# Kernel tuning notes

Hardware: AMD Instinct MI355X
Metric: run time of the kernel (lower is better)

Reference implementation:

```python
import jax, jax.numpy as jnp
import numpy as np

E = 128   # embedding_dim
H = 4     # num_heads
D = E * H # internal width = 512 (MHA head_dim = E)
B = 512
N = 128


def setup_inputs() -> dict:
    key = jax.random.key(0)
    ks = jax.random.split(key, 16)
    s = lambda fan_in: 1.0 / np.sqrt(fan_in)
    u = lambda k, shape, sc: jax.random.uniform(k, shape, jnp.float32, -sc, sc)
    inp = {
        "x": jax.random.normal(ks[0], (B, N, E), jnp.float32),
        "weights": jax.random.uniform(ks[1], (B, N, 1), jnp.float32),
        # self.embedding: Linear(E, D)
        "emb_W": u(ks[2], (D, E), s(E)), "emb_b": u(ks[3], (D,), s(E)),
        # outer W_q/W_k/W_v: Linear(D, D)
        "wq_W": u(ks[4], (D, D), s(D)), "wq_b": u(ks[5], (D,), s(D)),
        "wk_W": u(ks[6], (D, D), s(D)), "wk_b": u(ks[7], (D,), s(D)),
        "wv_W": u(ks[8], (D, D), s(D)), "wv_b": u(ks[9], (D,), s(D)),
        # nn.MultiheadAttention packed in-projection (out_proj is irrelevant:
        # its output is discarded, only att_weights are used)
        "in_proj_W": u(ks[10], (3 * D, D), s(D)),
        "in_proj_b": jnp.zeros((3 * D,), jnp.float32),
        # LayerNorm(D)
        "ln_g": jnp.ones((D,), jnp.float32), "ln_b": jnp.zeros((D,), jnp.float32),
        # self.out: Linear(D, E)
        "out_W": u(ks[11], (E, D), s(D)), "out_b": u(ks[12], (E,), s(D)),
    }
    return inp


def reference(x, weights, emb_W, emb_b, wq_W, wq_b, wk_W, wk_b, wv_W, wv_b,
              in_proj_W, in_proj_b, ln_g, ln_b, out_W, out_b):
    # x: [B, N, E] -> embedded [B, N, D]
    xe = x @ emb_W.T + emb_b
    # key_padding_mask: rows of xe that are all-zero
    pad = jnp.sum(jnp.abs(xe), axis=-1) == 0.0              # [B, N] bool

    # outer projections
    q_in = xe @ wq_W.T + wq_b
    k_in = xe @ wk_W.T + wk_b
    v_in = xe @ wv_W.T + wv_b                               # [B, N, D]

    # MHA internal packed in-projection
    Wq, Wk, Wv = in_proj_W[:D], in_proj_W[D:2 * D], in_proj_W[2 * D:]
    bq, bk, bv = in_proj_b[:D], in_proj_b[D:2 * D], in_proj_b[2 * D:]
    hd = D // H  # head_dim = E
    to_heads = lambda t: t.reshape(t.shape[0], t.shape[1], H, hd).transpose(0, 2, 1, 3)
    q = to_heads(q_in @ Wq.T + bq)                          # [B, H, N, hd]
    k = to_heads(k_in @ Wk.T + bk)

    scores = jnp.einsum('bhie,bhje->bhij', q, k) / jnp.sqrt(jnp.float32(hd))
    scores = jnp.where(pad[:, None, None, :], -jnp.inf, scores)
    attn = jax.nn.softmax(scores, axis=-1)                  # [B, H, N, N]
    att_weights = jnp.mean(attn, axis=1)                    # averaged over heads [B, N, N]

    # external reweighting + renormalization
    att_weights = att_weights * jnp.swapaxes(weights, -2, -1)  # [B,N,N]*[B,1,N]
    att_weights = att_weights / jnp.sum(att_weights, axis=-1, keepdims=True)

    # re-apply to outer V projection (MHA's own output is discarded)
    att_output = jnp.einsum('bij,bjd->bid', att_weights, v_in)

    h = xe + jax.nn.softplus(att_output)
    mu = jnp.mean(h, axis=-1, keepdims=True)
    var = jnp.mean((h - mu) ** 2, axis=-1, keepdims=True)
    h = (h - mu) / jnp.sqrt(var + 1e-5) * ln_g + ln_b
    return h @ out_W.T + out_b                              # [B, N, E]
```

## Files before the change

### kernel.cpp

```cpp
#include <hip/hip_runtime.h>
#include <stdint.h>


typedef __attribute__((ext_vector_type(8))) __bf16 bf16x8;
typedef __attribute__((ext_vector_type(8))) uint16_t u16x8;
typedef __attribute__((ext_vector_type(4))) float f32x4;

__device__ __forceinline__ float b2f(uint16_t h) {
  union { uint32_t u; float f; } c; c.u = ((uint32_t)h) << 16; return c.f;
}
__device__ __forceinline__ uint16_t f2b(float f) {
  union { float f; uint32_t u; } c; c.f = f;
  return (uint16_t)((c.u + 0x7fffu + ((c.u >> 16) & 1u)) >> 16);
}
__device__ __forceinline__ void gld16(void* lds, const void* g) {
  __builtin_amdgcn_global_load_lds(
      (const __attribute__((address_space(1))) uint32_t*)(g),
      (__attribute__((address_space(3))) uint32_t*)(lds),
      16, 0, 0);
}

#define MFMA16(a, b, c) __builtin_amdgcn_mfma_f32_16x16x32_bf16((a), (b), (c), 0, 0, 0)

__global__ __launch_bounds__(256) void pack_bf16(const float* __restrict__ in,
                                                 uint16_t* __restrict__ out, int n4) {
  int i = blockIdx.x * 256 + threadIdx.x;
  if (i >= n4) return;
  float4 v = ((const float4*)in)[i];
  ushort4 o;
  o.x = f2b(v.x); o.y = f2b(v.y); o.z = f2b(v.z); o.w = f2b(v.w);
  ((ushort4*)out)[i] = o;
}

__global__ __launch_bounds__(256) void pack_w6(
    const float* __restrict__ emb_W, const float* __restrict__ wq_W,
    const float* __restrict__ wk_W, const float* __restrict__ wv_W,
    const float* __restrict__ ipW, const float* __restrict__ out_W,
    uint16_t* __restrict__ embW2, uint16_t* __restrict__ wqW_bf,
    uint16_t* __restrict__ wkW_bf, uint16_t* __restrict__ Wvc,
    uint16_t* __restrict__ ip_bf, uint16_t* __restrict__ owW_bf) {
  int i = blockIdx.x * 256 + threadIdx.x;
  const float* src; uint16_t* dst; int off;
  if (i < 16384)       { src = emb_W; dst = embW2;  off = i; }
  else if (i < 81920)  { src = wq_W;  dst = wqW_bf; off = i - 16384; }
  else if (i < 147456) { src = wk_W;  dst = wkW_bf; off = i - 81920; }
  else if (i < 212992) { src = wv_W;  dst = Wvc;    off = i - 147456; }
  else if (i < 344064) { src = ipW;   dst = ip_bf;  off = i - 212992; }
  else if (i < 360448) { src = out_W; dst = owW_bf; off = i - 344064; }
  else return;
  float4 v = ((const float4*)src)[off];
  ushort4 o;
  o.x = f2b(v.x); o.y = f2b(v.y); o.z = f2b(v.z); o.w = f2b(v.w);
  ((ushort4*)dst)[off] = o;
}

__global__ __launch_bounds__(256) void bias_stage1(
    const float* __restrict__ wq_W, const float* __restrict__ wk_W,
    const float* __restrict__ wv_W, const float* __restrict__ emb_b,
    const float* __restrict__ wq_b, const float* __restrict__ wk_b,
    const float* __restrict__ wv_b,
    float* __restrict__ t1q, float* __restrict__ t1k, float* __restrict__ bve,
    float* __restrict__ pad_init, float* __restrict__ biasE) {
  const int gid = blockIdx.x * 256 + threadIdx.x;
  if (gid < 65536) pad_init[gid] = 0.f;
  if (gid < 512) biasE[gid] = emb_b[gid];
  const int t = threadIdx.x, l = t & 63, w = t >> 6;
  const int sel = blockIdx.x >> 7;
  const int row = (blockIdx.x & 127) * 4 + w;
  const float* Wbig = sel == 0 ? wq_W : (sel == 1 ? wk_W : wv_W);
  const float* b2   = sel == 0 ? wq_b : (sel == 1 ? wk_b : wv_b);
  float* out        = sel == 0 ? t1q  : (sel == 1 ? t1k  : bve);
  float s = 0.f;
  #pragma unroll
  for (int j = 0; j < 8; ++j) {
    int c = j * 64 + l;
    s += Wbig[(size_t)row * 512 + c] * emb_b[c];
  }
  #pragma unroll
  for (int m = 1; m < 64; m <<= 1) s += __shfl_xor(s, m);
  if (l == 0) out[row] = s + b2[row];
}

__global__ __launch_bounds__(256) void bias_stage2(
    const float* __restrict__ ipW, const float* __restrict__ ipb,
    const float* __restrict__ t1q, const float* __restrict__ t1k,
    float* __restrict__ bqe, float* __restrict__ bke) {
  const int t = threadIdx.x, l = t & 63, w = t >> 6;
  const int sel = blockIdx.x >> 7;
  const int row = (blockIdx.x & 127) * 4 + w;
  const float* Wbig = ipW + (size_t)sel * 262144;
  const float* b1   = sel == 0 ? t1q : t1k;
  const float* b2   = ipb + sel * 512;
  float* out        = sel == 0 ? bqe : bke;
  float s = 0.f;
  #pragma unroll
  for (int j = 0; j < 8; ++j) {
    int c = j * 64 + l;
    s += Wbig[(size_t)row * 512 + c] * b1[c];
  }
  #pragma unroll
  for (int m = 1; m < 64; m <<= 1) s += __shfl_xor(s, m);
  if (l == 0) out[row] = s + b2[row];
}

template <int BIAS_MODE, bool PAD_ACC>
__global__ __launch_bounds__(256) void gemm_btp_kernel(
    const uint16_t* __restrict__ A, long long sA,
    const uint16_t* __restrict__ W, long long sW,
    const float* __restrict__ bias, long long sBias,
    uint16_t* __restrict__ C, long long sC,
    int mIter, float* __restrict__ padout) {
  __shared__ uint16_t Ws[2][128 * 64];
  __shared__ uint16_t As[2][128 * 64];
  const int t = threadIdx.x, l = t & 63, w = t >> 6;
  const int wr = w >> 1, wc = w & 1, l15 = l & 15, hi = l >> 4;
  const int gx = gridDim.x, gy = gridDim.y;
  const int nwg = gx * gy * gridDim.z;
  const int lin = blockIdx.x + gx * (blockIdx.y + gy * blockIdx.z);
  const int cpx = nwg >> 3;
  const int sw = (nwg & 7) ? lin : ((lin & 7) * cpx + (lin >> 3));
  const int ntile = sw % gx;
  const int rest = sw / gx;
  const int mg = rest % gy, bz = rest / gy;
  const uint16_t* Ab = A + (size_t)bz * sA;
  const uint16_t* Wb = W + (size_t)bz * sW;
  uint16_t* Cb = C + (size_t)bz * sC;
  const float* biasb = bias + (size_t)bz * sBias;
  const int srow = t >> 3;
  const int schunk = (t & 7) * 8;
  const int gchunk = (((t & 7) ^ (srow & 7)) * 8);
  const int rowB0 = ntile * 128;
  #pragma unroll
  for (int kt = 0; kt < 2; ++kt)
    #pragma unroll
    for (int i = 0; i < 4; ++i) {
      const int r = i * 32 + srow;
      gld16(&Ws[kt][r * 64 + schunk], Wb + (size_t)(rowB0 + r) * 128 + kt * 64 + gchunk);
    }
  auto stageA = [&](int u) {
    const int rowA0 = (mg * mIter + (u >> 1)) * 128;
    const int kb = (u & 1) << 6;
    #pragma unroll
    for (int i = 0; i < 4; ++i) {
      const int r = i * 32 + srow;
      gld16(&As[u & 1][r * 64 + schunk], Ab + (size_t)(rowA0 + r) * 128 + kb + gchunk);
    }
  };
  const int rsw = (l15 & 7);
  stageA(0);
  const int U = mIter * 2;
  f32x4 acc[4][4];
  for (int u = 0; u < U; ++u) {
    const int kt = u & 1;
    if (kt == 0) {
      #pragma unroll
      for (int m = 0; m < 4; ++m)
        #pragma unroll
        for (int n = 0; n < 4; ++n) acc[m][n] = (f32x4){0.f, 0.f, 0.f, 0.f};
    }
    if (u + 1 < U) {
      stageA(u + 1);
      asm volatile("s_waitcnt vmcnt(4)" ::: "memory");
    } else {
      asm volatile("s_waitcnt vmcnt(0)" ::: "memory");
    }
    __builtin_amdgcn_s_barrier();
    asm volatile("" ::: "memory");
    #pragma unroll
    for (int ks = 0; ks < 2; ++ks) {
      const int gck = ((ks * 4 + hi) ^ rsw) * 8;
      bf16x8 a[4], bb[4];
      #pragma unroll
      for (int m = 0; m < 4; ++m)
        a[m] = *(const bf16x8*)&As[kt][(wr * 64 + m * 16 + l15) * 64 + gck];
      #pragma unroll
      for (int n = 0; n < 4; ++n)
        bb[n] = *(const bf16x8*)&Ws[kt][(wc * 64 + n * 16 + l15) * 64 + gck];
      #pragma unroll
      for (int m = 0; m < 4; ++m)
        #pragma unroll
        for (int n = 0; n < 4; ++n) acc[m][n] = MFMA16(a[m], bb[n], acc[m][n]);
    }
    asm volatile("" ::: "memory");
    __builtin_amdgcn_s_barrier();
    if (kt == 1) {
      const int rowA0 = (mg * mIter + (u >> 1)) * 128;
      #pragma unroll
      for (int m = 0; m < 4; ++m) {
        const int row = rowA0 + wr * 64 + m * 16 + hi * 4;
        float padp[4] = {0.f, 0.f, 0.f, 0.f};
        #pragma unroll
        for (int n = 0; n < 4; ++n) {
          const int col = rowB0 + wc * 64 + n * 16 + l15;
          float bv = 0.f;
          if constexpr (BIAS_MODE == 1) bv = biasb[col];
          #pragma unroll
          for (int r = 0; r < 4; ++r) {
            float rv = acc[m][n][r] + bv;
            if constexpr (PAD_ACC) padp[r] += fabsf(rv);
            Cb[(size_t)(row + r) * 512 + col] = f2b(rv);
          }
        }
        if constexpr (PAD_ACC) {
          if (bz == 0) {
            #pragma unroll
            for (int r = 0; r < 4; ++r) {
              float s2 = padp[r];
              s2 += __shfl_xor(s2, 1); s2 += __shfl_xor(s2, 2);
              s2 += __shfl_xor(s2, 4); s2 += __shfl_xor(s2, 8);
              if (l15 == 0) atomicAdd(padout + row + r, s2);
            }
          }
        }
      }
    }
  }
}

template <typename OT, int BIAS_MODE>
__global__ __launch_bounds__(256) void gemm_bt_kernel(
    const uint16_t* __restrict__ A, long long sA,
    const uint16_t* __restrict__ W, long long sW,
    const float* __restrict__ bias, long long sBias,
    OT* __restrict__ C, long long sC, int N, int K) {
  __shared__ uint16_t As[2][128 * 64];
  __shared__ uint16_t Bs[2][128 * 64];
  const int t = threadIdx.x, l = t & 63, w = t >> 6;
  const int wr = w >> 1, wc = w & 1, l15 = l & 15, hi = l >> 4;
  const int gx = gridDim.x, gy = gridDim.y;
  const int nwg = gx * gy * gridDim.z;
  const int lin = blockIdx.x + gx * (blockIdx.y + gy * blockIdx.z);
  const int cpx = nwg >> 3;
  const int sw = (nwg & 7) ? lin : ((lin & 7) * cpx + (lin >> 3));
  const int ntile = sw % gx;
  const int rest = sw / gx;
  const int mtile = rest % gy, bz = rest / gy;
  const uint16_t* Ab = A + (size_t)bz * sA;
  const uint16_t* Wb = W + (size_t)bz * sW;
  OT* Cb = C + (size_t)bz * sC;
  const float* biasb = bias + (size_t)bz * sBias;
  f32x4 acc[4][4];
  #pragma unroll
  for (int m = 0; m < 4; ++m)
    #pragma unroll
    for (int n = 0; n < 4; ++n) acc[m][n] = (f32x4){0.f, 0.f, 0.f, 0.f};
  const int srow = t >> 3;
  const int schunk = (t & 7) * 8;
  const int gchunk = (((t & 7) ^ (srow & 7)) * 8);
  const int nk = K >> 6;
  const int rowA0 = mtile * 128, rowB0 = ntile * 128;
  auto stage = [&](int kt, int buf) {
    const int kb = kt << 6;
    #pragma unroll
    for (int i = 0; i < 4; ++i) {
      const int r = i * 32 + srow;
      gld16(&As[buf][r * 64 + schunk], Ab + (size_t)(rowA0 + r) * K + kb + gchunk);
      gld16(&Bs[buf][r * 64 + schunk], Wb + (size_t)(rowB0 + r) * K + kb + gchunk);
    }
  };
  stage(0, 0);
  const int rsw = (l15 & 7);
  for (int kt = 0; kt < nk; ++kt) {
    const int cur = kt & 1;
    if (kt + 1 < nk) {
      stage(kt + 1, cur ^ 1);
      asm volatile("s_waitcnt vmcnt(8)" ::: "memory");
    } else {
      asm volatile("s_waitcnt vmcnt(0)" ::: "memory");
    }
    __builtin_amdgcn_s_barrier();
    asm volatile("" ::: "memory");
    #pragma unroll
    for (int ks = 0; ks < 2; ++ks) {
      const int gck = ((ks * 4 + hi) ^ rsw) * 8;
      bf16x8 a[4], bb[4];
      #pragma unroll
      for (int m = 0; m < 4; ++m)
        a[m] = *(const bf16x8*)&As[cur][(wr * 64 + m * 16 + l15) * 64 + gck];
      #pragma unroll
      for (int n = 0; n < 4; ++n)
        bb[n] = *(const bf16x8*)&Bs[cur][(wc * 64 + n * 16 + l15) * 64 + gck];
      #pragma unroll
      for (int m = 0; m < 4; ++m)
        #pragma unroll
        for (int n = 0; n < 4; ++n) acc[m][n] = MFMA16(a[m], bb[n], acc[m][n]);
    }
    asm volatile("" ::: "memory");
    __builtin_amdgcn_s_barrier();
  }
  #pragma unroll
  for (int m = 0; m < 4; ++m) {
    const int row = rowA0 + wr * 64 + m * 16 + hi * 4;
    #pragma unroll
    for (int n = 0; n < 4; ++n) {
      const int col = rowB0 + wc * 64 + n * 16 + l15;
      float bv = 0.f;
      if constexpr (BIAS_MODE == 1) bv = biasb[col];
      #pragma unroll
      for (int r = 0; r < 4; ++r) {
        float rv = acc[m][n][r] + bv;
        if constexpr (sizeof(OT) == 2) {
          ((uint16_t*)Cb)[(size_t)(row + r) * N + col] = f2b(rv);
        } else {
          Cb[(size_t)(row + r) * N + col] = rv;
        }
      }
    }
  }
}

__global__ __launch_bounds__(256) void gemm_tx_kernel(
    const uint16_t* __restrict__ A, const uint16_t* __restrict__ B,
    uint16_t* __restrict__ C) {
  __shared__ uint16_t As[128 * 64];
  __shared__ uint16_t Bt[128 * 64];
  const int t = threadIdx.x, l = t & 63, w = t >> 6;
  const int wr = w >> 1, wc = w & 1, l15 = l & 15, hi = l >> 4;
  const int nwg = gridDim.x;
  const int lin = blockIdx.x;
  const int cpx = nwg >> 3;
  const int bz = (nwg & 7) ? lin : ((lin & 7) * cpx + (lin >> 3));
  const uint16_t* Ab = A + (size_t)bz * 16384;
  const uint16_t* Bb = B + (size_t)bz * 16384;
  uint16_t* Cb = C + (size_t)bz * 16384;
  f32x4 acc[4][4];
  #pragma unroll
  for (int m = 0; m < 4; ++m)
    #pragma unroll
    for (int n = 0; n < 4; ++n) acc[m][n] = (f32x4){0.f, 0.f, 0.f, 0.f};
  const int srow = t >> 3;
  const int schunk = (t & 7) * 8;
  const int gchunk = (((t & 7) ^ (srow & 7)) * 8);
  const int rsw = (l15 & 7);
  for (int kt = 0; kt < 2; ++kt) {
    const int kb = kt << 6;
    #pragma unroll
    for (int i = 0; i < 4; ++i) {
      const int r = i * 32 + srow;
      gld16(&As[r * 64 + schunk], Ab + (size_t)r * 128 + kb + gchunk);
    }
    #pragma unroll
    for (int rd = 0; rd < 4; ++rd) {
      const int id = rd * 256 + t;
      const int kr = id >> 4;
      const int c = (id & 15) * 8;
      u16x8 gv = *(const u16x8*)(Bb + (size_t)(kb + kr) * 128 + c);
      #pragma unroll
      for (int j = 0; j < 8; ++j) {
        const int row = c + j;
        const int sxz = (((row & 7) ^ ((row >> 3) & 7)) << 3);
        Bt[row * 64 + (kr ^ sxz)] = gv[j];
      }
    }
    __syncthreads();
    #pragma unroll
    for (int ks = 0; ks < 2; ++ks) {
      const int gck = ((ks * 4 + hi) ^ rsw) * 8;
      bf16x8 a[4], bb[4];
      #pragma unroll
      for (int m = 0; m < 4; ++m)
        a[m] = *(const bf16x8*)&As[(wr * 64 + m * 16 + l15) * 64 + gck];
      #pragma unroll
      for (int n = 0; n < 4; ++n) {
        const int nr = wc * 64 + n * 16 + l15;
        const int sxz = (((nr & 7) ^ ((nr >> 3) & 7)) << 3);
        const int bck = ((ks * 32 + hi * 8) ^ sxz);
        bb[n] = *(const bf16x8*)&Bt[nr * 64 + bck];
      }
      #pragma unroll
      for (int m = 0; m < 4; ++m)
        #pragma unroll
        for (int n = 0; n < 4; ++n) acc[m][n] = MFMA16(a[m], bb[n], acc[m][n]);
    }
    __syncthreads();
  }
  #pragma unroll
  for (int m = 0; m < 4; ++m) {
    const int row = wr * 64 + m * 16 + hi * 4;
    #pragma unroll
    for (int n = 0; n < 4; ++n) {
      const int col = wc * 64 + n * 16 + l15;
      #pragma unroll
      for (int r = 0; r < 4; ++r)
        Cb[(size_t)(row + r) * 128 + col] = f2b(acc[m][n][r]);
    }
  }
}

__global__ __launch_bounds__(256) void gemm_ab_kernel(
    const uint16_t* __restrict__ A, int lda, long long sA,
    const uint16_t* __restrict__ B, int ldb, long long sB,
    uint16_t* __restrict__ C, int ldc, long long sC, int K) {
  __shared__ uint16_t As[128 * 64];
  __shared__ uint16_t Bt[128 * 64];
  const int t = threadIdx.x, l = t & 63, w = t >> 6;
  const int wr = w >> 1, wc = w & 1, l15 = l & 15, hi = l >> 4;
  const int gx = gridDim.x, gy = gridDim.y;
  const int nwg = gx * gy * gridDim.z;
  const int lin = blockIdx.x + gx * (blockIdx.y + gy * blockIdx.z);
  const int cpx = nwg >> 3;
  const int sw = (nwg & 7) ? lin : ((lin & 7) * cpx + (lin >> 3));
  const int ntile = sw % gx;
  const int rest = sw / gx;
  const int mtile = rest % gy, bz = rest / gy;
  const uint16_t* Ab = A + (size_t)bz * sA;
  const uint16_t* Bb = B + (size_t)bz * sB;
  uint16_t* Cb = C + (size_t)bz * sC;
  f32x4 acc[4][4];
  #pragma unroll
  for (int m = 0; m < 4; ++m)
    #pragma unroll
    for (int n = 0; n < 4; ++n) acc[m][n] = (f32x4){0.f, 0.f, 0.f, 0.f};
  const int srow = t >> 3, schunk = (t & 7) * 8;
  const int nk = K >> 6;
  for (int kt = 0; kt < nk; ++kt) {
    const int kb = kt << 6;
    #pragma unroll
    for (int i = 0; i < 4; ++i) {
      const int r = i * 32 + srow;
      gld16(&As[r * 64 + schunk], Ab + (size_t)(mtile * 128 + r) * lda + kb + schunk);
    }
    #pragma unroll
    for (int rd = 0; rd < 4; ++rd) {
      const int id = rd * 256 + t;
      const int kr = id >> 4;
      const int c = (id & 15) * 8;
      u16x8 gv = *(const u16x8*)(Bb + (size_t)(kb + kr) * ldb + ntile * 128 + c);
      #pragma unroll
      for (int j = 0; j < 8; ++j) Bt[(c + j) * 64 + kr] = gv[j];
    }
    __syncthreads();
    #pragma unroll
    for (int ks = 0; ks < 2; ++ks) {
      const int k0 = ks * 32 + hi * 8;
      bf16x8 a[4], bb[4];
      #pragma unroll
      for (int m = 0; m < 4; ++m) a[m] = *(const bf16x8*)&As[(wr * 64 + m * 16 + l15) * 64 + k0];
      #pragma unroll
      for (int n = 0; n < 4; ++n) bb[n] = *(const bf16x8*)&Bt[(wc * 64 + n * 16 + l15) * 64 + k0];
      #pragma unroll
      for (int m = 0; m < 4; ++m)
        #pragma unroll
        for (int n = 0; n < 4; ++n) acc[m][n] = MFMA16(a[m], bb[n], acc[m][n]);
    }
    __syncthreads();
  }
  #pragma unroll
  for (int m = 0; m < 4; ++m) {
    const int row = mtile * 128 + wr * 64 + m * 16 + hi * 4;
    #pragma unroll
    for (int n = 0; n < 4; ++n) {
      const int col = ntile * 128 + wc * 64 + n * 16 + l15;
      #pragma unroll
      for (int r = 0; r < 4; ++r)
        Cb[(size_t)(row + r) * ldc + col] = f2b(acc[m][n][r]);
    }
  }
}

__global__ __launch_bounds__(256) void gemm_atb_kernel(
    const uint16_t* __restrict__ Wke, const uint16_t* __restrict__ Wqe,
    const float* __restrict__ bqe, uint16_t* __restrict__ Wg,
    float* __restrict__ vh) {
  __shared__ uint16_t At[128 * 64];
  __shared__ uint16_t Bt[128 * 64];
  const int h = blockIdx.x;
  const int t = threadIdx.x, l = t & 63, w = t >> 6;
  const int wr = w >> 1, wc = w & 1, l15 = l & 15, hi = l >> 4;
  const uint16_t* A = Wke + (size_t)h * 16384;
  const uint16_t* B = Wqe + (size_t)h * 16384;
  f32x4 acc[4][4];
  #pragma unroll
  for (int m = 0; m < 4; ++m)
    #pragma unroll
    for (int n = 0; n < 4; ++n) acc[m][n] = (f32x4){0.f, 0.f, 0.f, 0.f};
  float vacc = 0.f;
  for (int kt = 0; kt < 2; ++kt) {
    const int kb = kt << 6;
    #pragma unroll
    for (int rd = 0; rd < 4; ++rd) {
      const int id = rd * 256 + t;
      const int kr = id >> 4;
      const int c = (id & 15) * 8;
      u16x8 ga = *(const u16x8*)(A + (size_t)(kb + kr) * 128 + c);
      u16x8 gb = *(const u16x8*)(B + (size_t)(kb + kr) * 128 + c);
      #pragma unroll
      for (int j = 0; j < 8; ++j) {
        const int row = c + j;
        const int sxz = (((row & 7) ^ ((row >> 3) & 7)) << 3);
        At[row * 64 + (kr ^ sxz)] = ga[j];
        Bt[row * 64 + (kr ^ sxz)] = gb[j];
      }
    }
    __syncthreads();
    if (t < 128) {
      const int sxz = (((t & 7) ^ ((t >> 3) & 7)) << 3);
      for (int o = 0; o < 64; ++o)
        vacc += b2f(At[t * 64 + (o ^ sxz)]) * bqe[h * 128 + kb + o];
    }
    #pragma unroll
    for (int ks = 0; ks < 2; ++ks) {
      bf16x8 a[4], bb[4];
      #pragma unroll
      for (int m = 0; m < 4; ++m) {
        const int mr = wr * 64 + m * 16 + l15;
        const int sxz = (((mr & 7) ^ ((mr >> 3) & 7)) << 3);
        a[m] = *(const bf16x8*)&At[mr * 64 + ((ks * 32 + hi * 8) ^ sxz)];
      }
      #pragma unroll
      for (int n = 0; n < 4; ++n) {
        const int nr = wc * 64 + n * 16 + l15;
        const int sxz = (((nr & 7) ^ ((nr >> 3) & 7)) << 3);
        bb[n] = *(const bf16x8*)&Bt[nr * 64 + ((ks * 32 + hi * 8) ^ sxz)];
      }
      #pragma unroll
      for (int m = 0; m < 4; ++m)
        #pragma unroll
        for (int n = 0; n < 4; ++n) acc[m][n] = MFMA16(a[m], bb[n], acc[m][n]);
    }
    __syncthreads();
  }
  if (t < 128) vh[h * 128 + t] = vacc;
  #pragma unroll
  for (int m = 0; m < 4; ++m) {
    const int row = wr * 64 + m * 16 + hi * 4;
    #pragma unroll
    for (int n = 0; n < 4; ++n) {
      const int col = wc * 64 + n * 16 + l15;
      #pragma unroll
      for (int r = 0; r < 4; ++r)
        Wg[(size_t)h * 16384 + (size_t)(row + r) * 128 + col] = f2b(acc[m][n][r]);
    }
  }
}

__global__ __launch_bounds__(512) void att_fused(
    const uint16_t* __restrict__ xg, const uint16_t* __restrict__ Wg,
    const float* __restrict__ vh, const float* __restrict__ wts,
    const float* __restrict__ padsum, uint16_t* __restrict__ aw) {
  __shared__ uint16_t Xr[2][128 * 64];
  __shared__ uint16_t GP[2][128 * 64];
  __shared__ float bS[4][128];
  const int blk = blockIdx.x;
  const int b = (blk & 7) * 64 + (blk >> 3);
  const int t = threadIdx.x, l = t & 63, wband = t >> 6;
  const int l15 = l & 15, hi = l >> 4;
  const int srow = t >> 3;
  const int schunk = (t & 7) * 8;
  const int gchunk = (((t & 7) ^ (srow & 7)) * 8);
  const float SCALE = 0.088388347648318447f;
  const int rsw = (l15 & 7);

  const uint16_t* xb = xg + (size_t)b * 16384;
  #pragma unroll
  for (int kt = 0; kt < 2; ++kt)
    #pragma unroll
    for (int i = 0; i < 2; ++i) {
      const int r = i * 64 + srow;
      gld16(&Xr[kt][r * 64 + schunk], xb + (size_t)r * 128 + kt * 64 + gchunk);
      gld16(&GP[kt][r * 64 + schunk], Wg + (size_t)r * 128 + kt * 64 + gchunk);
    }
  asm volatile("s_waitcnt vmcnt(0)" ::: "memory");
  __builtin_amdgcn_s_barrier();
  {
    const int hh = t >> 7, j = t & 127;
    float s = 0.f;
    for (int e = 0; e < 128; ++e) {
      const int c = e & 63;
      const int addr = j * 64 + ((((c >> 3) ^ (j & 7)) << 3) | (c & 7));
      s += b2f(Xr[e >> 6][addr]) * vh[hh * 128 + e];
    }
    bS[hh][j] = s * SCALE +
                ((padsum[(size_t)b * 128 + j] == 0.f) ? -__builtin_inff() : 0.f);
  }

  f32x4 awacc[8];
  #pragma unroll
  for (int n = 0; n < 8; ++n) awacc[n] = (f32x4){0.f, 0.f, 0.f, 0.f};
  u16x8 wreg[4];

  for (int h = 0; h < 4; ++h) {
    f32x4 pacc[8];
    #pragma unroll
    for (int n = 0; n < 8; ++n) pacc[n] = (f32x4){0.f, 0.f, 0.f, 0.f};
    __builtin_amdgcn_s_setprio(1);
    #pragma unroll
    for (int kt = 0; kt < 2; ++kt)
      #pragma unroll
      for (int ks = 0; ks < 2; ++ks) {
        const int gck = ((ks * 4 + hi) ^ rsw) * 8;
        bf16x8 a, bb[8];
        a = *(const bf16x8*)&Xr[kt][(wband * 16 + l15) * 64 + gck];
        #pragma unroll
        for (int n = 0; n < 8; ++n)
          bb[n] = *(const bf16x8*)&GP[kt][(n * 16 + l15) * 64 + gck];
        #pragma unroll
        for (int n = 0; n < 8; ++n) pacc[n] = MFMA16(a, bb[n], pacc[n]);
      }
    __builtin_amdgcn_s_setprio(0);
    if (h + 1 < 4) {
      #pragma unroll
      for (int kt = 0; kt < 2; ++kt)
        #pragma unroll
        for (int i = 0; i < 2; ++i) {
          const int r = i * 64 + srow;
          wreg[kt * 2 + i] = *(const u16x8*)(Wg + (size_t)(h + 1) * 16384 +
                                             (size_t)r * 128 + kt * 64 + gchunk);
        }
    }
    __builtin_amdgcn_s_barrier();
    #pragma unroll
    for (int n = 0; n < 8; ++n) {
      const int cl = n * 16 + l15;
      const int c = cl & 63;
      #pragma unroll
      for (int r = 0; r < 4; ++r) {
        const int rr = wband * 16 + hi * 4 + r;
        GP[cl >> 6][rr * 64 + ((((c >> 3) ^ (rr & 7)) << 3) | (c & 7))] =
            f2b(pacc[n][r]);
      }
    }
    __builtin_amdgcn_s_barrier();
    f32x4 sacc[8];
    #pragma unroll
    for (int n = 0; n < 8; ++n) sacc[n] = (f32x4){0.f, 0.f, 0.f, 0.f};
    __builtin_amdgcn_s_setprio(1);
    #pragma unroll
    for (int kt = 0; kt < 2; ++kt)
      #pragma unroll
      for (int ks = 0; ks < 2; ++ks) {
        const int gck = ((ks * 4 + hi) ^ rsw) * 8;
        bf16x8 a, bb[8];
        a = *(const bf16x8*)&GP[kt][(wband * 16 + l15) * 64 + gck];
        #pragma unroll
        for (int n = 0; n < 8; ++n)
          bb[n] = *(const bf16x8*)&Xr[kt][(n * 16 + l15) * 64 + gck];
        #pragma unroll
        for (int n = 0; n < 8; ++n) sacc[n] = MFMA16(a, bb[n], sacc[n]);
      }
    __builtin_amdgcn_s_setprio(0);
    #pragma unroll
    for (int r = 0; r < 4; ++r) {
      float e[8], z = 0.f;
      #pragma unroll
      for (int n = 0; n < 8; ++n) {
        e[n] = __expf(sacc[n][r] * SCALE + bS[h][n * 16 + l15]);
        z += e[n];
      }
      z += __shfl_xor(z, 1); z += __shfl_xor(z, 2);
      z += __shfl_xor(z, 4); z += __shfl_xor(z, 8);
      const float zi = 1.f / z;
      #pragma unroll
      for (int n = 0; n < 8; ++n) awacc[n][r] += e[n] * zi;
    }
    if (h + 1 < 4) {
      __builtin_amdgcn_s_barrier();
      asm volatile("s_waitcnt vmcnt(0)" ::: "memory");
      #pragma unroll
      for (int kt = 0; kt < 2; ++kt)
        #pragma unroll
        for (int i = 0; i < 2; ++i) {
          const int r = i * 64 + srow;
          *(u16x8*)&GP[kt][r * 64 + schunk] = wreg[kt * 2 + i];
        }
      __builtin_amdgcn_s_barrier();
    }
  }
  float wv[8];
  #pragma unroll
  for (int n = 0; n < 8; ++n) wv[n] = wts[(size_t)b * 128 + n * 16 + l15];
  #pragma unroll
  for (int r = 0; r < 4; ++r) {
    float z = 0.f;
    #pragma unroll
    for (int n = 0; n < 8; ++n) z += awacc[n][r] * wv[n];
    z += __shfl_xor(z, 1); z += __shfl_xor(z, 2);
    z += __shfl_xor(z, 4); z += __shfl_xor(z, 8);
    const float zi = 1.f / z;
    const int row = wband * 16 + hi * 4 + r;
    #pragma unroll
    for (int n = 0; n < 8; ++n) {
      const int col = n * 16 + l15;
      aw[(size_t)b * 16384 + (size_t)row * 128 + col] =
          f2b(awacc[n][r] * wv[n] * zi);
    }
  }
}

__global__ __launch_bounds__(256) void lnh_kernel(const uint16_t* __restrict__ xe,
                                                  const uint16_t* __restrict__ O,
                                                  const float* __restrict__ g,
                                                  const float* __restrict__ be,
                                                  uint16_t* __restrict__ hout) {
  const int t = threadIdx.x, l = t & 63, w = t >> 6;
  const size_t row = (size_t)blockIdx.x * 4 + w;
  const size_t base = row * 512 + l * 8;
  u16x8 xv = *(const u16x8*)(xe + base);
  u16x8 ov = *(const u16x8*)(O + base);
  float hv[8];
  #pragma unroll
  for (int j = 0; j < 8; ++j) {
    float o = b2f(ov[j]);
    float sp = fmaxf(o, 0.f) + __logf(1.f + __expf(-fabsf(o)));
    hv[j] = b2f(xv[j]) + sp;
  }
  float s = 0.f;
  #pragma unroll
  for (int j = 0; j < 8; ++j) s += hv[j];
  #pragma unroll
  for (int m = 1; m < 64; m <<= 1) s += __shfl_xor(s, m);
  const float mu = s * (1.f / 512.f);
  float vs = 0.f;
  #pragma unroll
  for (int j = 0; j < 8; ++j) { float d = hv[j] - mu; vs += d * d; }
  #pragma unroll
  for (int m = 1; m < 64; m <<= 1) vs += __shfl_xor(vs, m);
  const float rstd = rsqrtf(vs * (1.f / 512.f) + 1e-5f);
  u16x8 outv;
  #pragma unroll
  for (int j = 0; j < 8; ++j) {
    const int c = l * 8 + j;
    outv[j] = f2b((hv[j] - mu) * rstd * g[c] + be[c]);
  }
  *(u16x8*)(hout + base) = outv;
}

extern "C" void kernel_launch(void* const* d_in, const int* in_sizes, int n_in,
                              void* d_out, int out_size, void* d_ws, size_t ws_size,
                              hipStream_t stream) {
  (void)in_sizes; (void)n_in; (void)out_size; (void)ws_size;
  const float* x     = (const float*)d_in[0];
  const float* wts   = (const float*)d_in[1];
  const float* emb_W = (const float*)d_in[2];
  const float* emb_b = (const float*)d_in[3];
  const float* wq_W  = (const float*)d_in[4];
  const float* wq_b  = (const float*)d_in[5];
  const float* wk_W  = (const float*)d_in[6];
  const float* wk_b  = (const float*)d_in[7];
  const float* wv_W  = (const float*)d_in[8];
  const float* wv_b  = (const float*)d_in[9];
  const float* ipW   = (const float*)d_in[10];
  const float* ipb   = (const float*)d_in[11];
  const float* ln_g  = (const float*)d_in[12];
  const float* ln_b  = (const float*)d_in[13];
  const float* out_W = (const float*)d_in[14];
  const float* out_b = (const float*)d_in[15];

  char* ws = (char*)d_ws;
  size_t off = 0;
  auto alloc = [&](size_t bytes) { void* p = ws + off; off += (bytes + 255) & ~(size_t)255; return p; };
  uint16_t* wqW_bf = (uint16_t*)alloc(524288);
  uint16_t* wkW_bf = (uint16_t*)alloc(524288);
  uint16_t* ip_bf  = (uint16_t*)alloc(1048576);
  uint16_t* owW_bf = (uint16_t*)alloc(131072);
  uint16_t* Wqc    = (uint16_t*)alloc(524288);
  uint16_t* Wkc    = (uint16_t*)alloc(524288);
  uint16_t* Wvc    = (uint16_t*)alloc(524288);
  uint16_t* embW2  = (uint16_t*)alloc(131072);
  uint16_t* Wqe    = (uint16_t*)alloc(131072);
  uint16_t* Wke    = (uint16_t*)alloc(131072);
  uint16_t* Wve    = (uint16_t*)alloc(131072);
  uint16_t* Wg     = (uint16_t*)alloc(131072);
  float*    vhbuf  = (float*)alloc(2048);
  float*    t1q    = (float*)alloc(2048);
  float*    t1k    = (float*)alloc(2048);
  float*    biasE  = (float*)alloc(2048);
  float*    bqe    = (float*)alloc(2048);
  float*    bke    = (float*)alloc(2048);
  float*    bve    = (float*)alloc(2048);
  float*    pad    = (float*)alloc(262144);
  uint16_t* xe     = (uint16_t*)alloc(67108864);
  uint16_t* B1     = (uint16_t*)alloc(67108864);
  uint16_t* B2     = (uint16_t*)alloc(67108864);

  uint16_t* aw   = (uint16_t*)d_out;
  uint16_t* x_bf = (uint16_t*)d_out + 8388608;
  uint16_t* tb   = B1;
  uint16_t* Ob   = B2;
  uint16_t* hb   = B1;

  const int TB = 256;
  pack_bf16<<<8192, TB, 0, stream>>>(x, x_bf, 2097152);
  pack_w6<<<1408, TB, 0, stream>>>(emb_W, wq_W, wk_W, wv_W, ipW, out_W,
                                   embW2, wqW_bf, wkW_bf, Wvc, ip_bf, owW_bf);
  bias_stage1<<<384, TB, 0, stream>>>(wq_W, wk_W, wv_W, emb_b, wq_b, wk_b, wv_b,
                                      t1q, t1k, bve, pad, biasE);
  bias_stage2<<<256, TB, 0, stream>>>(ipW, ipb, t1q, t1k, bqe, bke);
  gemm_ab_kernel<<<dim3(4, 4, 2), TB, 0, stream>>>(ip_bf, 512, 262144, wqW_bf, 512, 262144,
                                                   Wqc, 512, 262144, 512);
  gemm_ab_kernel<<<dim3(1, 4, 3), TB, 0, stream>>>(Wqc, 512, 262144, embW2, 128, 0,
                                                   Wqe, 128, 65536, 512);
  gemm_atb_kernel<<<4, TB, 0, stream>>>(Wke, Wqe, bqe, Wg, vhbuf);
  gemm_btp_kernel<1, true><<<dim3(4, 128, 1), TB, 0, stream>>>(
      x_bf, 0, embW2, 0, biasE, 0, xe, 0, 4, pad);
  att_fused<<<512, 512, 0, stream>>>(x_bf, Wg, vhbuf, wts, pad, aw);
  gemm_tx_kernel<<<512, TB, 0, stream>>>(aw, x_bf, tb);
  gemm_btp_kernel<1, false><<<dim3(4, 128, 1), TB, 0, stream>>>(
      tb, 0, Wve, 0, bve, 0, Ob, 0, 4, nullptr);
  lnh_kernel<<<16384, TB, 0, stream>>>(xe, Ob, ln_g, ln_b, hb);
  gemm_bt_kernel<float, 1><<<dim3(1, 512, 1), TB, 0, stream>>>(
      hb, 0, owW_bf, 0, out_b, 0, (float*)d_out, 0, 128, 512);
}
```

Measured before the change: 237.6 us.

## Fuse attention-weights times X product into att_fused kernel, drop gemm_tx

```diff
diff --git a/kernel.cpp b/kernel.cpp
--- a/kernel.cpp
+++ b/kernel.cpp
@@ -309,84 +309,6 @@
   }
 }
 
-__global__ __launch_bounds__(256) void gemm_tx_kernel(
-    const uint16_t* __restrict__ A, const uint16_t* __restrict__ B,
-    uint16_t* __restrict__ C) {
-  __shared__ uint16_t As[128 * 64];
-  __shared__ uint16_t Bt[128 * 64];
-  const int t = threadIdx.x, l = t & 63, w = t >> 6;
-  const int wr = w >> 1, wc = w & 1, l15 = l & 15, hi = l >> 4;
-  const int nwg = gridDim.x;
-  const int lin = blockIdx.x;
-  const int cpx = nwg >> 3;
-  const int bz = (nwg & 7) ? lin : ((lin & 7) * cpx + (lin >> 3));
-  const uint16_t* Ab = A + (size_t)bz * 16384;
-  const uint16_t* Bb = B + (size_t)bz * 16384;
-  uint16_t* Cb = C + (size_t)bz * 16384;
-  f32x4 acc[4][4];
-  #pragma unroll
-  for (int m = 0; m < 4; ++m)
-    #pragma unroll
-    for (int n = 0; n < 4; ++n) acc[m][n] = (f32x4){0.f, 0.f, 0.f, 0.f};
-  const int srow = t >> 3;
-  const int schunk = (t & 7) * 8;
-  const int gchunk = (((t & 7) ^ (srow & 7)) * 8);
-  const int rsw = (l15 & 7);
-  for (int kt = 0; kt < 2; ++kt) {
-    const int kb = kt << 6;
-    #pragma unroll
-    for (int i = 0; i < 4; ++i) {
-      const int r = i * 32 + srow;
-      gld16(&As[r * 64 + schunk], Ab + (size_t)r * 128 + kb + gchunk);
-    }
-    #pragma unroll
-    for (int rd = 0; rd < 4; ++rd) {
-      const int id = rd * 256 + t;
-      const int kr = id >> 4;
-      const int c = (id & 15) * 8;
-      u16x8 gv = *(const u16x8*)(Bb + (size_t)(kb + kr) * 128 + c);
-      #pragma unroll
-      for (int j = 0; j < 8; ++j) {
-        const int row = c + j;
-        const int sxz = (((row & 7) ^ ((row >> 3) & 7)) << 3);
-        Bt[row * 64 + (kr ^ sxz)] = gv[j];
-      }
-    }
-    __syncthreads();
-    #pragma unroll
-    for (int ks = 0; ks < 2; ++ks) {
-      const int gck = ((ks * 4 + hi) ^ rsw) * 8;
-      bf16x8 a[4], bb[4];
-      #pragma unroll
-      for (int m = 0; m < 4; ++m)
-        a[m] = *(const bf16x8*)&As[(wr * 64 + m * 16 + l15) * 64 + gck];
-      #pragma unroll
-      for (int n = 0; n < 4; ++n) {
-        const int nr = wc * 64 + n * 16 + l15;
-        const int sxz = (((nr & 7) ^ ((nr >> 3) & 7)) << 3);
-        const int bck = ((ks * 32 + hi * 8) ^ sxz);
-        bb[n] = *(const bf16x8*)&Bt[nr * 64 + bck];
-      }
-      #pragma unroll
-      for (int m = 0; m < 4; ++m)
-        #pragma unroll
-        for (int n = 0; n < 4; ++n) acc[m][n] = MFMA16(a[m], bb[n], acc[m][n]);
-    }
-    __syncthreads();
-  }
-  #pragma unroll
-  for (int m = 0; m < 4; ++m) {
-    const int row = wr * 64 + m * 16 + hi * 4;
-    #pragma unroll
-    for (int n = 0; n < 4; ++n) {
-      const int col = wc * 64 + n * 16 + l15;
-      #pragma unroll
-      for (int r = 0; r < 4; ++r)
-        Cb[(size_t)(row + r) * 128 + col] = f2b(acc[m][n][r]);
-    }
-  }
-}
-
 __global__ __launch_bounds__(256) void gemm_ab_kernel(
     const uint16_t* __restrict__ A, int lda, long long sA,
     const uint16_t* __restrict__ B, int ldb, long long sB,
@@ -537,7 +459,7 @@
 __global__ __launch_bounds__(512) void att_fused(
     const uint16_t* __restrict__ xg, const uint16_t* __restrict__ Wg,
     const float* __restrict__ vh, const float* __restrict__ wts,
-    const float* __restrict__ padsum, uint16_t* __restrict__ aw) {
+    const float* __restrict__ padsum, uint16_t* __restrict__ tout) {
   __shared__ uint16_t Xr[2][128 * 64];
   __shared__ uint16_t GP[2][128 * 64];
   __shared__ float bS[4][128];
@@ -578,6 +500,7 @@
   #pragma unroll
   for (int n = 0; n < 8; ++n) awacc[n] = (f32x4){0.f, 0.f, 0.f, 0.f};
   u16x8 wreg[4];
+  u16x8 xtr[4];
 
   for (int h = 0; h < 4; ++h) {
     f32x4 pacc[8];
@@ -639,6 +562,15 @@
         for (int n = 0; n < 8; ++n) sacc[n] = MFMA16(a, bb[n], sacc[n]);
       }
     __builtin_amdgcn_s_setprio(0);
+    if (h == 3) {
+      #pragma unroll
+      for (int i = 0; i < 4; ++i) {
+        const int id = i * 512 + t;
+        const int jr = id >> 4;
+        const int cc = (id & 15) * 8;
+        xtr[i] = *(const u16x8*)(xb + (size_t)jr * 128 + cc);
+      }
+    }
     #pragma unroll
     for (int r = 0; r < 4; ++r) {
       float e[8], z = 0.f;
@@ -669,6 +601,7 @@
   float wv[8];
   #pragma unroll
   for (int n = 0; n < 8; ++n) wv[n] = wts[(size_t)b * 128 + n * 16 + l15];
+  __builtin_amdgcn_s_barrier();
   #pragma unroll
   for (int r = 0; r < 4; ++r) {
     float z = 0.f;
@@ -677,12 +610,58 @@
     z += __shfl_xor(z, 1); z += __shfl_xor(z, 2);
     z += __shfl_xor(z, 4); z += __shfl_xor(z, 8);
     const float zi = 1.f / z;
+    const int rr = wband * 16 + hi * 4 + r;
+    #pragma unroll
+    for (int n = 0; n < 8; ++n) {
+      const int cl = n * 16 + l15;
+      const int c = cl & 63;
+      GP[cl >> 6][rr * 64 + ((((c >> 3) ^ (rr & 7)) << 3) | (c & 7))] =
+          f2b(awacc[n][r] * wv[n] * zi);
+    }
+  }
+  asm volatile("s_waitcnt vmcnt(0)" ::: "memory");
+  #pragma unroll
+  for (int i = 0; i < 4; ++i) {
+    const int id = i * 512 + t;
+    const int jr = id >> 4;
+    const int cc = (id & 15) * 8;
+    const int kt2 = jr >> 6, kr = jr & 63;
+    #pragma unroll
+    for (int j = 0; j < 8; ++j) {
+      const int drow = cc + j;
+      const int sxz = (((drow & 7) ^ ((drow >> 3) & 7)) << 3);
+      Xr[kt2][drow * 64 + (kr ^ sxz)] = xtr[i][j];
+    }
+  }
+  __builtin_amdgcn_s_barrier();
+  f32x4 tacc[8];
+  #pragma unroll
+  for (int n = 0; n < 8; ++n) tacc[n] = (f32x4){0.f, 0.f, 0.f, 0.f};
+  __builtin_amdgcn_s_setprio(1);
+  #pragma unroll
+  for (int kt = 0; kt < 2; ++kt)
+    #pragma unroll
+    for (int ks = 0; ks < 2; ++ks) {
+      const int gck = ((ks * 4 + hi) ^ rsw) * 8;
+      bf16x8 a, bb[8];
+      a = *(const bf16x8*)&GP[kt][(wband * 16 + l15) * 64 + gck];
+      #pragma unroll
+      for (int n = 0; n < 8; ++n) {
+        const int nr = n * 16 + l15;
+        const int sxz = (((nr & 7) ^ ((nr >> 3) & 7)) << 3);
+        bb[n] = *(const bf16x8*)&Xr[kt][nr * 64 + ((ks * 32 + hi * 8) ^ sxz)];
+      }
+      #pragma unroll
+      for (int n = 0; n < 8; ++n) tacc[n] = MFMA16(a, bb[n], tacc[n]);
+    }
+  __builtin_amdgcn_s_setprio(0);
+  #pragma unroll
+  for (int r = 0; r < 4; ++r) {
     const int row = wband * 16 + hi * 4 + r;
     #pragma unroll
     for (int n = 0; n < 8; ++n) {
       const int col = n * 16 + l15;
-      aw[(size_t)b * 16384 + (size_t)row * 128 + col] =
-          f2b(awacc[n][r] * wv[n] * zi);
+      tout[(size_t)b * 16384 + (size_t)row * 128 + col] = f2b(tacc[n][r]);
     }
   }
 }
@@ -773,7 +752,6 @@
   uint16_t* B1     = (uint16_t*)alloc(67108864);
   uint16_t* B2     = (uint16_t*)alloc(67108864);
 
-  uint16_t* aw   = (uint16_t*)d_out;
   uint16_t* x_bf = (uint16_t*)d_out + 8388608;
   uint16_t* tb   = B1;
   uint16_t* Ob   = B2;
@@ -793,8 +771,7 @@
   gemm_atb_kernel<<<4, TB, 0, stream>>>(Wke, Wqe, bqe, Wg, vhbuf);
   gemm_btp_kernel<1, true><<<dim3(4, 128, 1), TB, 0, stream>>>(
       x_bf, 0, embW2, 0, biasE, 0, xe, 0, 4, pad);
-  att_fused<<<512, 512, 0, stream>>>(x_bf, Wg, vhbuf, wts, pad, aw);
-  gemm_tx_kernel<<<512, TB, 0, stream>>>(aw, x_bf, tb);
+  att_fused<<<512, 512, 0, stream>>>(x_bf, Wg, vhbuf, wts, pad, tb);
   gemm_btp_kernel<1, false><<<dim3(4, 128, 1), TB, 0, stream>>>(
       tb, 0, Wve, 0, bve, 0, Ob, 0, 4, nullptr);
   lnh_kernel<<<16384, TB, 0, stream>>>(xe, Ob, ln_g, ln_b, hb);
```

Result: faster. 232.2 us (-2.3%).
